# Optimization experiments

Measured on AMD Instinct MI355X. Metric: run time of the kernel, lower is better.

The kernel has to match this reference:

```python
import jax, jax.numpy as jnp
import numpy as np

L, N, C = 128, 32, 128
DIM_MLP, OUT = 128, 128


def setup_inputs() -> dict:
    key = jax.random.key(0)
    ks = jax.random.split(key, 6)
    s_in2 = 1.0 / np.sqrt(2 * C)
    s_mid = 1.0 / np.sqrt(DIM_MLP)
    s_in = 1.0 / np.sqrt(C)
    return {
        "x": jax.random.normal(ks[0], (L, N, C), jnp.float32),
        "attn_w1": jax.random.normal(ks[1], (2 * C, DIM_MLP), jnp.float32) * s_in2,
        "attn_b1": jnp.zeros((DIM_MLP,), jnp.float32),
        "attn_w2": jax.random.normal(ks[2], (DIM_MLP, OUT), jnp.float32) * s_mid,
        "attn_b2": jnp.zeros((OUT,), jnp.float32),
        "value_w1": jax.random.normal(ks[3], (C, DIM_MLP), jnp.float32) * s_in,
        "value_b1": jnp.zeros((DIM_MLP,), jnp.float32),
        "value_w2": jax.random.normal(ks[4], (DIM_MLP, OUT), jnp.float32) * s_mid,
        "value_b2": jnp.zeros((OUT,), jnp.float32),
    }


def reference(x, attn_w1, attn_b1, attn_w2, attn_b2,
              value_w1, value_b1, value_w2, value_b2):
    l, n, c = x.shape
    # Outer concat: pair[i, j, b] = concat(x[i, b], x[j, b])  -> (l, l, N, 2C)
    xi = jnp.broadcast_to(x[:, None, :, :], (l, l, n, c))
    xj = jnp.broadcast_to(x[None, :, :, :], (l, l, n, c))
    pair = jnp.concatenate([xi, xj], axis=-1)
    # Pairwise attention MLP (ReLU hidden, linear output)
    h = jax.nn.relu(pair @ attn_w1 + attn_b1)          # (l, l, N, dim_mlp)
    attn = h @ attn_w2 + attn_b2                       # (l, l, N, out)
    # Value MLP
    hv = jax.nn.relu(x @ value_w1 + value_b1)          # (l, N, dim_mlp)
    value = hv @ value_w2 + value_b2                   # (l, N, out)
    # Elementwise weighted reduce over key axis j (NOT a matmul over channels)
    out = jnp.einsum('ijbc,jbc->ibc', attn, value)     # (l, N, out)
    return out
```

## Files before the change

kernel.cpp:

```cpp
#include <hip/hip_runtime.h>
#include <hip/hip_bf16.h>

#define L_DIM 128
#define N_DIM 32
#define C_DIM 128
#define K_DIM 128
#define OUT_DIM 128

typedef __attribute__((ext_vector_type(8))) short short8;
typedef __attribute__((ext_vector_type(4))) float float4v;

static __device__ __forceinline__ short bf16_bits(float f) {
    __bf16 h = (__bf16)f;
    return __builtin_bit_cast(short, h);
}

static __device__ __forceinline__ void gl_lds16(const float* g, float* l) {
    __builtin_amdgcn_global_load_lds(
        (const __attribute__((address_space(1))) unsigned int*)g,
        (__attribute__((address_space(3))) unsigned int*)l, 16, 0, 0);
}

__global__ __launch_bounds__(256) void k_pre(
    const float* __restrict__ x,
    const float* __restrict__ attn_w1, const float* __restrict__ attn_b1,
    const float* __restrict__ attn_w2,
    const float* __restrict__ value_w1, const float* __restrict__ value_b1,
    const float* __restrict__ value_w2, const float* __restrict__ value_b2,
    float* __restrict__ P, float* __restrict__ Q, float* __restrict__ Vt,
    short* __restrict__ W2s)
{
    int bid = blockIdx.x;
    if (bid >= 512) {
        int e = (bid - 512) * 256 + threadIdx.x;
        int idx  = e & 7;
        int colr = (e >> 3) & 15;
        int quad = (e >> 7) & 3;
        int mi   = (e >> 9) & 3;
        int ct   = e >> 11;
        int k = quad * 8 + 32 * mi + idx;
        int c = ct * 16 + colr;
        W2s[e] = bf16_bits(attn_w2[k * OUT_DIM + c]);
        return;
    }

    __shared__ float xs[8][C_DIM];
    __shared__ float hvs[8][K_DIM];
    int tid = threadIdx.x;
    int b   = bid >> 4;
    int i0g = (bid & 15) * 8;

    {
        int f = tid * 4;
        int row = f >> 7, c = f & 127;
        *(float4v*)(&xs[row][c]) =
            *(const float4v*)(x + ((size_t)(i0g + row) * N_DIM + b) * C_DIM + c);
    }
    __syncthreads();

    int ks   = tid & 127;
    int half = tid >> 7;

    float pacc[4] = {0,0,0,0};
    float qacc[4] = {0,0,0,0};
    float hacc[4] = {0,0,0,0};
    #pragma unroll 4
    for (int c = 0; c < C_DIM; ++c) {
        float wa = attn_w1[c * K_DIM + ks];
        float wb = attn_w1[(C_DIM + c) * K_DIM + ks];
        float wv = value_w1[c * K_DIM + ks];
        #pragma unroll
        for (int r = 0; r < 4; ++r) {
            float xr = xs[half * 4 + r][c];
            pacc[r] = fmaf(xr, wa, pacc[r]);
            qacc[r] = fmaf(xr, wb, qacc[r]);
            hacc[r] = fmaf(xr, wv, hacc[r]);
        }
    }
    float b1 = attn_b1[ks], vb1 = value_b1[ks];
    #pragma unroll
    for (int r = 0; r < 4; ++r) {
        int i = i0g + half * 4 + r;
        P[((size_t)b * L_DIM + i) * K_DIM + ks] = pacc[r];
        Q[((size_t)b * L_DIM + i) * K_DIM + ks] = qacc[r] + b1;
        hvs[half * 4 + r][ks] = fmaxf(hacc[r] + vb1, 0.f);
    }
    __syncthreads();

    float vacc[4] = {0,0,0,0};
    #pragma unroll 4
    for (int k = 0; k < K_DIM; ++k) {
        float w = value_w2[k * OUT_DIM + ks];
        #pragma unroll
        for (int r = 0; r < 4; ++r)
            vacc[r] = fmaf(hvs[half * 4 + r][k], w, vacc[r]);
    }
    float vb2 = value_b2[ks];
    float4v vout = { vacc[0] + vb2, vacc[1] + vb2, vacc[2] + vb2, vacc[3] + vb2 };
    *(float4v*)(Vt + ((size_t)b * OUT_DIM + ks) * L_DIM + i0g + half * 4) = vout;
}

__global__ __launch_bounds__(256)
__attribute__((amdgpu_waves_per_eu(3)))
void k_main(
    const float* __restrict__ P, const float* __restrict__ Q,
    const float* __restrict__ Vt,
    const short* __restrict__ W2s, const float* __restrict__ attn_b2,
    float* __restrict__ out)
{
    __shared__ float Q_lds[2][16 * 128];
    __shared__ float V_lds[2][128 * 16];
    __shared__ float P_lds[4 * 128];

    int b    = blockIdx.x >> 5;
    int it4  = blockIdx.x & 31;
    int tid  = threadIdx.x;
    int wave = tid >> 6;
    int lane = tid & 63;
    int quad = lane >> 4;
    int col  = lane & 15;
    int ip   = wave >> 1;
    int cth  = wave & 1;

    const float* Qbase = Q  + (size_t)b * L_DIM * K_DIM;
    const float* Vbase = Vt + (size_t)b * OUT_DIM * L_DIM;

    short8 bfrag[4][4];
    const short8* w2p = (const short8*)W2s;
    #pragma unroll
    for (int cl = 0; cl < 4; ++cl)
        #pragma unroll
        for (int mi = 0; mi < 4; ++mi)
            bfrag[cl][mi] =
                w2p[(((cth * 4 + cl) * 4 + mi) * 4 + quad) * 16 + col];

    int qinv[2], vinv[2];
    #pragma unroll
    for (int t = 0; t < 2; ++t) {
        int n  = wave * 128 + t * 64 + lane;
        int j  = n >> 5, c16 = n & 31;
        int s8 = c16 >> 1, e = c16 & 1;
        int g  = s8 ^ (j & 7);
        qinv[t] = j * K_DIM + g * 8 + e * 4;
        int c  = n >> 2, s = n & 3;
        int ch = s ^ (c & 3);
        vinv[t] = c * L_DIM + ch * 4;
    }

    #pragma unroll
    for (int t = 0; t < 2; ++t) {
        gl_lds16(Qbase + qinv[t], &Q_lds[0][wave * 512 + t * 256]);
        gl_lds16(Vbase + vinv[t], &V_lds[0][wave * 512 + t * 256]);
    }
    if (wave == 0) {
        #pragma unroll
        for (int t = 0; t < 2; ++t) {
            int n = t * 64 + lane;
            gl_lds16(P + ((size_t)b * L_DIM + it4 * 4 + (n >> 5)) * K_DIM
                       + (n & 31) * 4,
                     &P_lds[t * 256]);
        }
    }
    __syncthreads();

    float acc0[4] = {0.f, 0.f, 0.f, 0.f};
    float acc1[4] = {0.f, 0.f, 0.f, 0.f};
    float sv[4]   = {0.f, 0.f, 0.f, 0.f};
    int pofs = 0;

    #pragma unroll 1
    for (int r = 0; r < 8; ++r) {
        int cur = r & 1;
        asm volatile("" : "+v"(pofs));

        if (r < 7) {
            int nxt = cur ^ 1;
            #pragma unroll
            for (int t = 0; t < 2; ++t) {
                gl_lds16(Qbase + qinv[t] + (r + 1) * 16 * K_DIM,
                         &Q_lds[nxt][wave * 512 + t * 256]);
                gl_lds16(Vbase + vinv[t] + (r + 1) * 16,
                         &V_lds[nxt][wave * 512 + t * 256]);
            }
        }

        short8 af[2][4];
        const float* Qrow = &Q_lds[cur][col * 128];
        const float* Prow = &P_lds[(ip * 2) * 128 + quad * 8 + pofs];
        #pragma unroll
        for (int ksl = 0; ksl < 4; ++ksl) {
            int s8 = (ksl * 4 + quad) ^ (col & 7);
            float4v q0 = *(const float4v*)(Qrow + s8 * 8);
            float4v q1 = *(const float4v*)(Qrow + s8 * 8 + 4);
            #pragma unroll
            for (int ii = 0; ii < 2; ++ii) {
                const float* Pc = Prow + ii * 128 + ksl * 32;
                float4v s0 = *(const float4v*)Pc + q0;
                float4v s1 = *(const float4v*)(Pc + 4) + q1;
                short8 a;
                #pragma unroll
                for (int t = 0; t < 4; ++t) {
                    a[t]     = bf16_bits(fmaxf(s0[t], 0.f));
                    a[t + 4] = bf16_bits(fmaxf(s1[t], 0.f));
                }
                af[ii][ksl] = a;
            }
        }

        #pragma unroll
        for (int cl = 0; cl < 4; ++cl) {
            float4v c40 = {0.f, 0.f, 0.f, 0.f};
            float4v c41 = {0.f, 0.f, 0.f, 0.f};
            #pragma unroll
            for (int ksl = 0; ksl < 4; ++ksl) {
                c40 = __builtin_amdgcn_mfma_f32_16x16x32_bf16(
                        af[0][ksl], bfrag[cl][ksl], c40, 0, 0, 0);
                c41 = __builtin_amdgcn_mfma_f32_16x16x32_bf16(
                        af[1][ksl], bfrag[cl][ksl], c41, 0, 0, 0);
            }
            int cc = cth * 64 + cl * 16 + col;
            float4v vv = *(const float4v*)
                (&V_lds[cur][cc * 16 + ((quad ^ (cc & 3)) << 2)]);
            #pragma unroll
            for (int rr = 0; rr < 4; ++rr) {
                acc0[cl] = fmaf(c40[rr], vv[rr], acc0[cl]);
                acc1[cl] = fmaf(c41[rr], vv[rr], acc1[cl]);
                sv[cl]  += vv[rr];
            }
        }

        if (r < 7) __syncthreads();
    }

    #pragma unroll
    for (int cl = 0; cl < 4; ++cl) {
        acc0[cl] += __shfl_xor(acc0[cl], 16, 64);
        acc0[cl] += __shfl_xor(acc0[cl], 32, 64);
        acc1[cl] += __shfl_xor(acc1[cl], 16, 64);
        acc1[cl] += __shfl_xor(acc1[cl], 32, 64);
        sv[cl]   += __shfl_xor(sv[cl], 16, 64);
        sv[cl]   += __shfl_xor(sv[cl], 32, 64);
    }

    if (quad == 0) {
        int i0 = it4 * 4 + ip * 2;
        #pragma unroll
        for (int cl = 0; cl < 4; ++cl) {
            int cc = cth * 64 + cl * 16 + col;
            float bsv = attn_b2[cc] * sv[cl];
            out[((size_t)i0 * N_DIM + b) * OUT_DIM + cc]       = acc0[cl] + bsv;
            out[((size_t)(i0 + 1) * N_DIM + b) * OUT_DIM + cc] = acc1[cl] + bsv;
        }
    }
}

extern "C" void kernel_launch(void* const* d_in, const int* in_sizes, int n_in,
                              void* d_out, int out_size, void* d_ws, size_t ws_size,
                              hipStream_t stream)
{
    const float* x        = (const float*)d_in[0];
    const float* attn_w1  = (const float*)d_in[1];
    const float* attn_b1  = (const float*)d_in[2];
    const float* attn_w2  = (const float*)d_in[3];
    const float* attn_b2  = (const float*)d_in[4];
    const float* value_w1 = (const float*)d_in[5];
    const float* value_b1 = (const float*)d_in[6];
    const float* value_w2 = (const float*)d_in[7];
    const float* value_b2 = (const float*)d_in[8];
    float* out = (float*)d_out;

    float* ws  = (float*)d_ws;
    float* P   = ws;
    float* Q   = ws + 524288;
    float* Vt  = ws + 1048576;
    short* W2s = (short*)(ws + 1572864);

    k_pre<<<576, 256, 0, stream>>>(x, attn_w1, attn_b1, attn_w2,
                                   value_w1, value_b1, value_w2, value_b2,
                                   P, Q, Vt, W2s);
    k_main<<<1024, 256, 0, stream>>>(P, Q, Vt, W2s, attn_b2, out);
}
```

Baseline: 124.6 us.

## Triple-buffer Q tiles and build next A-fragments ahead of MFMA

Result: no change. 124.4 us (-0.1%).

```diff
diff --git a/kernel.cpp b/kernel.cpp
--- a/kernel.cpp
+++ b/kernel.cpp
@@ -101,16 +101,16 @@
 }
 
 __global__ __launch_bounds__(256)
-__attribute__((amdgpu_waves_per_eu(3)))
+__attribute__((amdgpu_waves_per_eu(2)))
 void k_main(
     const float* __restrict__ P, const float* __restrict__ Q,
     const float* __restrict__ Vt,
     const short* __restrict__ W2s, const float* __restrict__ attn_b2,
     float* __restrict__ out)
 {
-    __shared__ float Q_lds[2][16 * 128];
-    __shared__ float V_lds[2][128 * 16];
-    __shared__ float P_lds[4 * 128];
+    __shared__ float Q_lds[3][2048];
+    __shared__ float V_lds[2][2048];
+    __shared__ float P_lds[512];
 
     int b    = blockIdx.x >> 5;
     int it4  = blockIdx.x & 31;
@@ -134,32 +134,35 @@
             bfrag[cl][mi] =
                 w2p[(((cth * 4 + cl) * 4 + mi) * 4 + quad) * 16 + col];
 
-    int qinv[2], vinv[2];
+    int qsrc[2], vsrc[2];
     #pragma unroll
     for (int t = 0; t < 2; ++t) {
-        int n  = wave * 128 + t * 64 + lane;
-        int j  = n >> 5, c16 = n & 31;
-        int s8 = c16 >> 1, e = c16 & 1;
-        int g  = s8 ^ (j & 7);
-        qinv[t] = j * K_DIM + g * 8 + e * 4;
-        int c  = n >> 2, s = n & 3;
-        int ch = s ^ (c & 3);
-        vinv[t] = c * L_DIM + ch * 4;
-    }
-
-    #pragma unroll
-    for (int t = 0; t < 2; ++t) {
-        gl_lds16(Qbase + qinv[t], &Q_lds[0][wave * 512 + t * 256]);
-        gl_lds16(Vbase + vinv[t], &V_lds[0][wave * 512 + t * 256]);
-    }
+        int n = (t * 4 + wave) * 64 + lane;
+        qsrc[t] = (n & 15) * K_DIM + (n >> 4) * 4;
+        int c = n >> 2, s = n & 3;
+        vsrc[t] = c * L_DIM + ((s ^ (c & 3)) << 2);
+    }
+
+    auto stageQ = [&](int jt, int buf) {
+        #pragma unroll
+        for (int t = 0; t < 2; ++t)
+            gl_lds16(Qbase + jt * 16 * K_DIM + qsrc[t],
+                     &Q_lds[buf][(t * 4 + wave) * 256]);
+    };
+    auto stageV = [&](int jt, int buf) {
+        #pragma unroll
+        for (int t = 0; t < 2; ++t)
+            gl_lds16(Vbase + jt * 16 + vsrc[t],
+                     &V_lds[buf][(t * 4 + wave) * 256]);
+    };
+
+    stageQ(0, 0);
+    stageQ(1, 1);
+    stageV(0, 0);
     if (wave == 0) {
-        #pragma unroll
-        for (int t = 0; t < 2; ++t) {
-            int n = t * 64 + lane;
-            gl_lds16(P + ((size_t)b * L_DIM + it4 * 4 + (n >> 5)) * K_DIM
-                       + (n & 31) * 4,
-                     &P_lds[t * 256]);
-        }
+        const float* Pbase = P + ((size_t)b * L_DIM + it4 * 4) * K_DIM;
+        gl_lds16(Pbase + lane * 4,       &P_lds[0]);
+        gl_lds16(Pbase + 256 + lane * 4, &P_lds[256]);
     }
     __syncthreads();
 
@@ -168,33 +171,19 @@
     float sv[4]   = {0.f, 0.f, 0.f, 0.f};
     int pofs = 0;
 
-    #pragma unroll 1
-    for (int r = 0; r < 8; ++r) {
-        int cur = r & 1;
-        asm volatile("" : "+v"(pofs));
-
-        if (r < 7) {
-            int nxt = cur ^ 1;
-            #pragma unroll
-            for (int t = 0; t < 2; ++t) {
-                gl_lds16(Qbase + qinv[t] + (r + 1) * 16 * K_DIM,
-                         &Q_lds[nxt][wave * 512 + t * 256]);
-                gl_lds16(Vbase + vinv[t] + (r + 1) * 16,
-                         &V_lds[nxt][wave * 512 + t * 256]);
-            }
-        }
-
-        short8 af[2][4];
-        const float* Qrow = &Q_lds[cur][col * 128];
-        const float* Prow = &P_lds[(ip * 2) * 128 + quad * 8 + pofs];
+    short8 af[2][2][4];
+
+    auto build = [&](int jt, int p) {
+        const float* qb = &Q_lds[jt % 3][col * 4];
+        const float* Pr = &P_lds[(ip * 2) * 128 + quad * 8 + pofs];
         #pragma unroll
         for (int ksl = 0; ksl < 4; ++ksl) {
-            int s8 = (ksl * 4 + quad) ^ (col & 7);
-            float4v q0 = *(const float4v*)(Qrow + s8 * 8);
-            float4v q1 = *(const float4v*)(Qrow + s8 * 8 + 4);
+            int kc0 = (ksl * 4 + quad) * 2;
+            float4v q0 = *(const float4v*)(qb + kc0 * 64);
+            float4v q1 = *(const float4v*)(qb + kc0 * 64 + 64);
             #pragma unroll
             for (int ii = 0; ii < 2; ++ii) {
-                const float* Pc = Prow + ii * 128 + ksl * 32;
+                const float* Pc = Pr + ii * 128 + ksl * 32;
                 float4v s0 = *(const float4v*)Pc + q0;
                 float4v s1 = *(const float4v*)(Pc + 4) + q1;
                 short8 a;
@@ -203,10 +192,22 @@
                     a[t]     = bf16_bits(fmaxf(s0[t], 0.f));
                     a[t + 4] = bf16_bits(fmaxf(s1[t], 0.f));
                 }
-                af[ii][ksl] = a;
+                af[p][ii][ksl] = a;
             }
         }
-
+    };
+
+    build(0, 0);
+
+    #pragma unroll
+    for (int r = 0; r < 8; ++r) {
+        asm volatile("" : "+v"(pofs));
+        if (r < 6) stageQ(r + 2, (r + 2) % 3);
+        if (r < 7) stageV(r + 1, (r + 1) & 1);
+
+        if (r < 7) build(r + 1, (r + 1) & 1);
+
+        const float* Vc = &V_lds[r & 1][0];
         #pragma unroll
         for (int cl = 0; cl < 4; ++cl) {
             float4v c40 = {0.f, 0.f, 0.f, 0.f};
@@ -214,13 +215,13 @@
             #pragma unroll
             for (int ksl = 0; ksl < 4; ++ksl) {
                 c40 = __builtin_amdgcn_mfma_f32_16x16x32_bf16(
-                        af[0][ksl], bfrag[cl][ksl], c40, 0, 0, 0);
+                        af[r & 1][0][ksl], bfrag[cl][ksl], c40, 0, 0, 0);
                 c41 = __builtin_amdgcn_mfma_f32_16x16x32_bf16(
-                        af[1][ksl], bfrag[cl][ksl], c41, 0, 0, 0);
+                        af[r & 1][1][ksl], bfrag[cl][ksl], c41, 0, 0, 0);
             }
             int cc = cth * 64 + cl * 16 + col;
             float4v vv = *(const float4v*)
-                (&V_lds[cur][cc * 16 + ((quad ^ (cc & 3)) << 2)]);
+                (Vc + cc * 16 + ((quad ^ (cc & 3)) << 2));
             #pragma unroll
             for (int rr = 0; rr < 4; ++rr) {
                 acc0[cl] = fmaf(c40[rr], vv[rr], acc0[cl]);
```
